# Optimization experiments

Measured on AMD Instinct MI355X. Metric: run time of the kernel, lower is better.

The kernel has to match this reference:

```python
import jax, jax.numpy as jnp
import numpy as np

N_NODES = 50000
N_EDGES = 1600000
NODE_DIM = 1024
HID = 128
OUT = 128
LN_EPS = 1e-5


def setup_inputs() -> dict:
    key = jax.random.key(0)
    ks = jax.random.split(key, 8)
    s = lambda d: 1.0 / np.sqrt(d)
    return {
        "x": jax.random.normal(ks[0], (N_NODES, NODE_DIM), jnp.float32),
        "edge_index": jax.random.randint(ks[1], (2, N_EDGES), 0, N_NODES, jnp.int64),
        "proj_w": jax.random.normal(ks[2], (HID, NODE_DIM), jnp.float32) * s(NODE_DIM),
        "proj_b": jnp.zeros((HID,), jnp.float32),
        "lin_l_w": jax.random.normal(ks[3], (HID, HID), jnp.float32) * s(HID),
        "lin_l_b": jnp.zeros((HID,), jnp.float32),
        "lin_r_w": jax.random.normal(ks[4], (HID, HID), jnp.float32) * s(HID),
        "ln_g": jnp.ones((HID,), jnp.float32),
        "ln_b": jnp.zeros((HID,), jnp.float32),
        "out_w": jax.random.normal(ks[5], (OUT, HID), jnp.float32) * s(HID),
        "out_b": jnp.zeros((OUT,), jnp.float32),
    }


def reference(x, edge_index, proj_w, proj_b, lin_l_w, lin_l_b, lin_r_w, ln_g, ln_b, out_w, out_b):
    n = x.shape[0]
    # input projection + ReLU: [N, node_dim] -> [N, H]
    h = jax.nn.relu(x @ proj_w.T + proj_b)
    # SAGEConv(mean): gather source features, mean-scatter to targets
    src, dst = edge_index[0], edge_index[1]
    agg = jax.ops.segment_sum(h[src], dst, num_segments=n)  # [N, H]
    deg = jax.ops.segment_sum(jnp.ones((src.shape[0],), h.dtype), dst, num_segments=n)
    mean_nbr = agg / jnp.maximum(deg, 1.0)[:, None]
    h = mean_nbr @ lin_l_w.T + lin_l_b + h @ lin_r_w.T
    # LayerNorm over feature dim
    mu = h.mean(-1, keepdims=True)
    var = jnp.mean((h - mu) ** 2, -1, keepdims=True)
    h = (h - mu) * jax.lax.rsqrt(var + LN_EPS) * ln_g + ln_b
    h = jax.nn.relu(h)  # dropout is identity in eval
    # batch=None -> global mean pool over all nodes: [1, H]
    g = h.mean(0, keepdims=True)
    return g @ out_w.T + out_b
```

## Files before the change

kernel.cpp:

```cpp
#include <hip/hip_runtime.h>

#define N_NODES  50000
#define N_EDGES  1600000
#define NODE_DIM 1024
#define HID      128
#define LN_EPS   1e-5f
#define NBUCK    196
#define SHARD    6250

typedef float f32x4 __attribute__((ext_vector_type(4)));
typedef __bf16 bf16x8 __attribute__((ext_vector_type(8)));
typedef unsigned short u16x8 __attribute__((ext_vector_type(8)));

__device__ __forceinline__ unsigned short f2bf(float f) {
  __bf16 b = (__bf16)f;
  return __builtin_bit_cast(unsigned short, b);
}
__device__ __forceinline__ unsigned int pkbf(float a, float b) {
  return (unsigned int)f2bf(a) | ((unsigned int)f2bf(b) << 16);
}
__device__ __forceinline__ float bf2f(unsigned short v) {
  return __uint_as_float((unsigned int)v << 16);
}

__device__ __forceinline__ int scan256_excl(int v, int buf[2][256], int t) {
  int cur = 0;
  buf[0][t] = v;
  __syncthreads();
  for (int off = 1; off < 256; off <<= 1) {
    int nxt = cur ^ 1;
    int s = buf[cur][t];
    if (t >= off) s += buf[cur][t - off];
    buf[nxt][t] = s;
    cur = nxt;
    __syncthreads();
  }
  return buf[cur][t] - v;
}

__global__ __launch_bounds__(256) void k_proj(const float* __restrict__ x,
                                              const float* __restrict__ pw,
                                              const float* __restrict__ pb,
                                              unsigned short* __restrict__ h) {
  __shared__ unsigned short As[2][128][32];
  __shared__ unsigned short Bs[2][128][32];
  const int tid = threadIdx.x;
  const int m0 = blockIdx.x * 128;
  const int wave = tid >> 6, lane = tid & 63;
  const int wm = (wave >> 1) * 64, wn = (wave & 1) * 64;
  const int srow = tid >> 1;
  const int sub  = tid & 1;
  const int fr = lane & 15, ko = (lane >> 4) * 8;

  f32x4 acc[4][4] = {};
  const int arow = m0 + srow;
  const bool aval = (arow < N_NODES);
  const float* xrow = x + (size_t)arow * NODE_DIM + sub * 32;
  const float* brow = pw + (size_t)srow * NODE_DIM + sub * 32;

  for (int k0 = 0; k0 < NODE_DIM; k0 += 64) {
    float4 av[8], bv[8];
    if (aval) {
      const float4* p = (const float4*)(xrow + k0);
#pragma unroll
      for (int j = 0; j < 8; j++) av[j] = p[j];
    } else {
#pragma unroll
      for (int j = 0; j < 8; j++) av[j] = make_float4(0.f, 0.f, 0.f, 0.f);
    }
    const float4* q = (const float4*)(brow + k0);
#pragma unroll
    for (int j = 0; j < 8; j++) bv[j] = q[j];

    __syncthreads();
    unsigned int* da = (unsigned int*)&As[sub][srow][0];
    unsigned int* db = (unsigned int*)&Bs[sub][srow][0];
#pragma unroll
    for (int j = 0; j < 8; j++) {
      da[2 * j]     = pkbf(av[j].x, av[j].y);
      da[2 * j + 1] = pkbf(av[j].z, av[j].w);
      db[2 * j]     = pkbf(bv[j].x, bv[j].y);
      db[2 * j + 1] = pkbf(bv[j].z, bv[j].w);
    }
    __syncthreads();

#pragma unroll
    for (int s = 0; s < 2; s++) {
      bf16x8 af[4], bfr[4];
#pragma unroll
      for (int m = 0; m < 4; m++)
        af[m] = *(const bf16x8*)&As[s][wm + m * 16 + fr][ko];
#pragma unroll
      for (int n = 0; n < 4; n++)
        bfr[n] = *(const bf16x8*)&Bs[s][wn + n * 16 + fr][ko];
#pragma unroll
      for (int m = 0; m < 4; m++)
#pragma unroll
        for (int n = 0; n < 4; n++)
          acc[m][n] = __builtin_amdgcn_mfma_f32_16x16x32_bf16(af[m], bfr[n], acc[m][n], 0, 0, 0);
    }
  }

  const int cr = (lane >> 4) * 4, cc = lane & 15;
#pragma unroll
  for (int n = 0; n < 4; n++) {
    const int col = wn + n * 16 + cc;
    const float bias = pb[col];
#pragma unroll
    for (int m = 0; m < 4; m++) {
#pragma unroll
      for (int i = 0; i < 4; i++) {
        const int row = m0 + wm + m * 16 + cr + i;
        if (row < N_NODES) {
          float v = acc[m][n][i] + bias;
          h[(size_t)row * HID + col] = f2bf(v > 0.f ? v : 0.f);
        }
      }
    }
  }
}

__global__ __launch_bounds__(256) void k_hist(const int* __restrict__ ei,
                                              int* __restrict__ counts) {
  __shared__ int bins[NBUCK];
  int t = threadIdx.x;
  if (t < NBUCK) bins[t] = 0;
  __syncthreads();
  int base = blockIdx.x * SHARD;
  for (int i = t; i < SHARD; i += 256)
    atomicAdd(&bins[ei[N_EDGES + base + i] >> 8], 1);
  __syncthreads();
  if (t < NBUCK) counts[t * 256 + blockIdx.x] = bins[t];
}

__global__ __launch_bounds__(256) void k_s1(const int* __restrict__ counts,
                                            int* __restrict__ basem,
                                            int* __restrict__ btot) {
  __shared__ int buf[2][256];
  int t = threadIdx.x, b = blockIdx.x;
  int v = counts[b * 256 + t];
  int excl = scan256_excl(v, buf, t);
  basem[b * 256 + t] = excl;
  if (t == 255) btot[b] = excl + v;
}

__global__ __launch_bounds__(256) void k_s2(const int* __restrict__ btot,
                                            int* __restrict__ bstart,
                                            float* __restrict__ accum) {
  __shared__ int buf[2][256];
  int t = threadIdx.x;
  int v = (t < NBUCK) ? btot[t] : 0;
  int excl = scan256_excl(v, buf, t);
  if (t < NBUCK) bstart[t] = excl;
  if (t == 0) bstart[NBUCK] = N_EDGES;
  if (t < HID) accum[t] = 0.f;
}

__global__ __launch_bounds__(256) void k_scatter(const int* __restrict__ ei,
                                                 const int* __restrict__ basem,
                                                 const int* __restrict__ bstart,
                                                 unsigned int* __restrict__ bs) {
  __shared__ int cur[NBUCK];
  int t = threadIdx.x;
  if (t < NBUCK) cur[t] = bstart[t] + basem[t * 256 + blockIdx.x];
  __syncthreads();
  int base = blockIdx.x * SHARD;
  for (int i = t; i < SHARD; i += 256) {
    int e = base + i;
    unsigned int src = (unsigned int)ei[e];
    unsigned int dst = (unsigned int)ei[N_EDGES + e];
    int pos = atomicAdd(&cur[dst >> 8], 1);
    bs[pos] = src | ((dst & 255u) << 16);
  }
}

__global__ __launch_bounds__(256) void k_bucket(const int* __restrict__ bstart,
                                                const unsigned int* __restrict__ bs,
                                                unsigned short* __restrict__ nbr,
                                                int* __restrict__ offs,
                                                int* __restrict__ deg) {
  __shared__ int bins[256];
  __shared__ int buf[2][256];
  __shared__ int curs[256];
  int t = threadIdx.x, b = blockIdx.x;
  int s = bstart[b], e = bstart[b + 1];
  bins[t] = 0;
  __syncthreads();
  for (int i = s + t; i < e; i += 256)
    atomicAdd(&bins[(bs[i] >> 16) & 255u], 1);
  __syncthreads();
  int v = bins[t];
  int excl = scan256_excl(v, buf, t);
  int node = b * 256 + t;
  deg[node]  = v;
  offs[node] = s + excl;
  curs[t]    = s + excl;
  __syncthreads();
  for (int i = s + t; i < e; i += 256) {
    unsigned int p = bs[i];
    int pos = atomicAdd(&curs[(p >> 16) & 255u], 1);
    nbr[pos] = (unsigned short)(p & 0xffffu);
  }
}

__global__ __launch_bounds__(256) void k_gather(const unsigned short* __restrict__ h,
                                                const unsigned short* __restrict__ nbr,
                                                const int* __restrict__ offs,
                                                const int* __restrict__ deg,
                                                unsigned short* __restrict__ mn) {
  const int wave = threadIdx.x >> 6;
  const int lane = threadIdx.x & 63;
  const int node = blockIdx.x * 4 + wave;
  if (node >= N_NODES) return;
  const int g = lane >> 4, li = lane & 15;
  const int d  = deg[node];
  const int st = offs[node];
  float a[8] = {0.f, 0.f, 0.f, 0.f, 0.f, 0.f, 0.f, 0.f};
  int n = g;
  for (; n + 4 < d; n += 8) {
    int s0 = nbr[st + n];
    int s1 = nbr[st + n + 4];
    u16x8 v0 = *(const u16x8*)(h + (size_t)s0 * HID + li * 8);
    u16x8 v1 = *(const u16x8*)(h + (size_t)s1 * HID + li * 8);
#pragma unroll
    for (int k = 0; k < 8; k++) a[k] += bf2f(v0[k]) + bf2f(v1[k]);
  }
  if (n < d) {
    int s0 = nbr[st + n];
    u16x8 v0 = *(const u16x8*)(h + (size_t)s0 * HID + li * 8);
#pragma unroll
    for (int k = 0; k < 8; k++) a[k] += bf2f(v0[k]);
  }
#pragma unroll
  for (int k = 0; k < 8; k++) {
    a[k] += __shfl_xor(a[k], 16);
    a[k] += __shfl_xor(a[k], 32);
  }
  if (g == 0) {
    float inv = 1.f / fmaxf((float)d, 1.f);
    u16x8 r;
#pragma unroll
    for (int k = 0; k < 8; k++) r[k] = f2bf(a[k] * inv);
    *(u16x8*)(mn + (size_t)node * HID + li * 8) = r;
  }
}

__global__ __launch_bounds__(256) void k_sage(const unsigned short* __restrict__ mn,
                                              const unsigned short* __restrict__ h,
                                              const float* __restrict__ wl,
                                              const float* __restrict__ wr,
                                              const float* __restrict__ lb,
                                              const float* __restrict__ lg,
                                              const float* __restrict__ lbt,
                                              float* __restrict__ accum) {
  __shared__ unsigned short As[128 * 32];
  __shared__ unsigned short Bs[128 * 32];
  __shared__ float T3[32 * 128];
  __shared__ float red[4][128];
  const int tid = threadIdx.x;
  const int m0 = blockIdx.x * 128;
  const int wave = tid >> 6, lane = tid & 63;
  const int wm = (wave >> 1) * 64, wn = (wave & 1) * 64;
  const int srow = tid >> 1, scol = (tid & 1) * 16;
  const int fr = lane & 15, ko = (lane >> 4) * 8;

  f32x4 acc[4][4] = {};

  for (int k0 = 0; k0 < 2 * HID; k0 += 32) {
    const unsigned short* baseA = (k0 < HID) ? mn : h;
    const float* baseB = (k0 < HID) ? wl : wr;
    const int kk = (k0 & (HID - 1)) + scol;
    const int arow = m0 + srow;
    u16x8 a0 = {0, 0, 0, 0, 0, 0, 0, 0}, a1 = a0;
    if (arow < N_NODES) {
      const u16x8* p = (const u16x8*)(baseA + (size_t)arow * HID + kk);
      a0 = p[0]; a1 = p[1];
    }
    const float4* q = (const float4*)(baseB + (size_t)srow * HID + kk);
    float4 b0 = q[0], b1 = q[1], b2 = q[2], b3 = q[3];

    __syncthreads();
    *(u16x8*)&As[srow * 32 + scol]     = a0;
    *(u16x8*)&As[srow * 32 + scol + 8] = a1;
    unsigned int* db = (unsigned int*)&Bs[srow * 32 + scol];
    db[0] = pkbf(b0.x, b0.y); db[1] = pkbf(b0.z, b0.w);
    db[2] = pkbf(b1.x, b1.y); db[3] = pkbf(b1.z, b1.w);
    db[4] = pkbf(b2.x, b2.y); db[5] = pkbf(b2.z, b2.w);
    db[6] = pkbf(b3.x, b3.y); db[7] = pkbf(b3.z, b3.w);
    __syncthreads();

    bf16x8 af[4], bfr[4];
#pragma unroll
    for (int m = 0; m < 4; m++)
      af[m] = *(const bf16x8*)&As[(wm + m * 16 + fr) * 32 + ko];
#pragma unroll
    for (int n = 0; n < 4; n++)
      bfr[n] = *(const bf16x8*)&Bs[(wn + n * 16 + fr) * 32 + ko];
#pragma unroll
    for (int m = 0; m < 4; m++)
#pragma unroll
      for (int n = 0; n < 4; n++)
        acc[m][n] = __builtin_amdgcn_mfma_f32_16x16x32_bf16(af[m], bfr[n], acc[m][n], 0, 0, 0);
  }

  const int cr = (lane >> 4) * 4, cc = lane & 15;
  const int p = wave >> 1;
  const float g0 = lg[lane], g1 = lg[lane + 64];
  const float t0 = lbt[lane], t1 = lbt[lane + 64];
  float ax = 0.f, ay = 0.f;
#pragma unroll
  for (int m = 0; m < 4; m++) {
    __syncthreads();
#pragma unroll
    for (int n = 0; n < 4; n++) {
      const int col = wn + n * 16 + cc;
      const float bias = lb[col];
#pragma unroll
      for (int i = 0; i < 4; i++)
        T3[(p * 16 + cr + i) * 128 + col] = acc[m][n][i] + bias;
    }
    __syncthreads();
    for (int r8 = 0; r8 < 8; r8++) {
      int q8 = wave * 8 + r8;
      int grow = m0 + (q8 >> 4) * 64 + m * 16 + (q8 & 15);
      float v0 = T3[q8 * 128 + lane];
      float v1 = T3[q8 * 128 + lane + 64];
      float sum = v0 + v1, ss = v0 * v0 + v1 * v1;
#pragma unroll
      for (int off = 32; off > 0; off >>= 1) {
        sum += __shfl_xor(sum, off);
        ss  += __shfl_xor(ss, off);
      }
      float mu  = sum * (1.f / HID);
      float var = ss * (1.f / HID) - mu * mu;
      float rinv = rsqrtf(var + LN_EPS);
      if (grow < N_NODES) {
        float y0 = (v0 - mu) * rinv * g0 + t0;
        float y1 = (v1 - mu) * rinv * g1 + t1;
        ax += fmaxf(y0, 0.f);
        ay += fmaxf(y1, 0.f);
      }
    }
  }
  red[wave][lane]      = ax;
  red[wave][lane + 64] = ay;
  __syncthreads();
  if (wave == 0) {
    float a  = red[0][lane] + red[1][lane] + red[2][lane] + red[3][lane];
    float bb = red[0][lane + 64] + red[1][lane + 64] + red[2][lane + 64] + red[3][lane + 64];
    atomicAdd(&accum[lane], a);
    atomicAdd(&accum[lane + 64], bb);
  }
}

__global__ __launch_bounds__(128) void k_final(const float* __restrict__ accum,
                                               const float* __restrict__ ow,
                                               const float* __restrict__ ob,
                                               float* __restrict__ out) {
  __shared__ float gs[HID];
  int t = threadIdx.x;
  gs[t] = accum[t] * (1.f / N_NODES);
  __syncthreads();
  float s = ob[t];
  for (int k = 0; k < HID; k++) s += gs[k] * ow[t * HID + k];
  out[t] = s;
}

extern "C" void kernel_launch(void* const* d_in, const int* in_sizes, int n_in,
                              void* d_out, int out_size, void* d_ws, size_t ws_size,
                              hipStream_t stream) {
  const float* x   = (const float*)d_in[0];
  const int*   ei  = (const int*)d_in[1];
  const float* pw  = (const float*)d_in[2];
  const float* pb  = (const float*)d_in[3];
  const float* wl  = (const float*)d_in[4];
  const float* lb  = (const float*)d_in[5];
  const float* wr  = (const float*)d_in[6];
  const float* lg  = (const float*)d_in[7];
  const float* lbt = (const float*)d_in[8];
  const float* ow  = (const float*)d_in[9];
  const float* ob  = (const float*)d_in[10];
  float* out = (float*)d_out;

  const int PAD = NBUCK * 256;
  unsigned short* h  = (unsigned short*)d_ws;
  unsigned short* mn = h + (size_t)PAD * HID;
  unsigned int* bsp  = (unsigned int*)(mn + (size_t)PAD * HID);
  unsigned short* nbr = (unsigned short*)(bsp + N_EDGES);
  int* counts = (int*)(nbr + N_EDGES);
  int* basem  = counts + NBUCK * 256;
  int* btot   = basem + NBUCK * 256;
  int* bstart = btot + 256;
  int* offs   = bstart + 256;
  int* deg    = offs + PAD;
  float* accum = (float*)(deg + PAD);

  const int MB = (N_NODES + 127) / 128;

  hipLaunchKernelGGL(k_proj,    dim3(MB),    dim3(256), 0, stream, x, pw, pb, h);
  hipLaunchKernelGGL(k_hist,    dim3(256),   dim3(256), 0, stream, ei, counts);
  hipLaunchKernelGGL(k_s1,      dim3(NBUCK), dim3(256), 0, stream, counts, basem, btot);
  hipLaunchKernelGGL(k_s2,      dim3(1),     dim3(256), 0, stream, btot, bstart, accum);
  hipLaunchKernelGGL(k_scatter, dim3(256),   dim3(256), 0, stream, ei, basem, bstart, bsp);
  hipLaunchKernelGGL(k_bucket,  dim3(NBUCK), dim3(256), 0, stream, bstart, bsp, nbr, offs, deg);
  hipLaunchKernelGGL(k_gather,  dim3((N_NODES + 3) / 4), dim3(256), 0, stream, h, nbr, offs, deg, mn);
  hipLaunchKernelGGL(k_sage,    dim3(MB),    dim3(256), 0, stream, mn, h, wl, wr, lb, lg, lbt, accum);
  hipLaunchKernelGGL(k_final,   dim3(1),     dim3(128), 0, stream, accum, ow, ob, out);
}
```

Baseline: 474.0 us.

## Pre-convert weights to bf16 and drop LDS staging in projection and SAGE GEMMs

Adds a prep kernel that converts the projection weight and the concatenated lin_l/lin_r weights to bf16 once per call. The projection and SAGE GEMMs now load MFMA fragments straight from global memory into registers, with each wave owning 32 rows by 128 columns, so the LDS staging and barriers go away. LayerNorm is computed in registers using shuffle reductions instead of an LDS transpose. The pooling atomics are replaced by per-block partial sums that k_final reduces. The risk is that each wave must fetch its whole B operand from L2 or L1 with no LDS sharing, and x rows are loaded as narrower 32-byte pieces per lane.

```diff
diff --git a/kernel.cpp b/kernel.cpp
--- a/kernel.cpp
+++ b/kernel.cpp
@@ -7,6 +7,7 @@
 #define LN_EPS   1e-5f
 #define NBUCK    196
 #define SHARD    6250
+#define MB       391
 
 typedef float f32x4 __attribute__((ext_vector_type(4)));
 typedef __bf16 bf16x8 __attribute__((ext_vector_type(8)));
@@ -21,6 +22,12 @@
 }
 __device__ __forceinline__ float bf2f(unsigned short v) {
   return __uint_as_float((unsigned int)v << 16);
+}
+__device__ __forceinline__ bf16x8 cvt8(const float4 a, const float4 b) {
+  union { unsigned int u[4]; bf16x8 v; } t;
+  t.u[0] = pkbf(a.x, a.y); t.u[1] = pkbf(a.z, a.w);
+  t.u[2] = pkbf(b.x, b.y); t.u[3] = pkbf(b.z, b.w);
+  return t.v;
 }
 
 __device__ __forceinline__ int scan256_excl(int v, int buf[2][256], int t) {
@@ -38,82 +45,75 @@
   return buf[cur][t] - v;
 }
 
+__global__ __launch_bounds__(256) void k_prep(const float* __restrict__ pw,
+                                              const float* __restrict__ wl,
+                                              const float* __restrict__ wr,
+                                              unsigned short* __restrict__ pwb,
+                                              unsigned short* __restrict__ wcomb) {
+  int i = blockIdx.x * 256 + threadIdx.x;
+  if (i < HID * NODE_DIM) {
+    pwb[i] = f2bf(pw[i]);
+  } else {
+    int j = i - HID * NODE_DIM;
+    if (j < HID * 256) {
+      int c = j >> 8, k = j & 255;
+      float v = (k < HID) ? wl[c * HID + k] : wr[c * HID + (k - HID)];
+      wcomb[j] = f2bf(v);
+    }
+  }
+}
+
 __global__ __launch_bounds__(256) void k_proj(const float* __restrict__ x,
-                                              const float* __restrict__ pw,
+                                              const unsigned short* __restrict__ pwb,
                                               const float* __restrict__ pb,
                                               unsigned short* __restrict__ h) {
-  __shared__ unsigned short As[2][128][32];
-  __shared__ unsigned short Bs[2][128][32];
-  const int tid = threadIdx.x;
-  const int m0 = blockIdx.x * 128;
-  const int wave = tid >> 6, lane = tid & 63;
-  const int wm = (wave >> 1) * 64, wn = (wave & 1) * 64;
-  const int srow = tid >> 1;
-  const int sub  = tid & 1;
-  const int fr = lane & 15, ko = (lane >> 4) * 8;
-
-  f32x4 acc[4][4] = {};
-  const int arow = m0 + srow;
-  const bool aval = (arow < N_NODES);
-  const float* xrow = x + (size_t)arow * NODE_DIM + sub * 32;
-  const float* brow = pw + (size_t)srow * NODE_DIM + sub * 32;
-
-  for (int k0 = 0; k0 < NODE_DIM; k0 += 64) {
-    float4 av[8], bv[8];
-    if (aval) {
-      const float4* p = (const float4*)(xrow + k0);
-#pragma unroll
-      for (int j = 0; j < 8; j++) av[j] = p[j];
-    } else {
-#pragma unroll
-      for (int j = 0; j < 8; j++) av[j] = make_float4(0.f, 0.f, 0.f, 0.f);
-    }
-    const float4* q = (const float4*)(brow + k0);
-#pragma unroll
-    for (int j = 0; j < 8; j++) bv[j] = q[j];
-
-    __syncthreads();
-    unsigned int* da = (unsigned int*)&As[sub][srow][0];
-    unsigned int* db = (unsigned int*)&Bs[sub][srow][0];
-#pragma unroll
-    for (int j = 0; j < 8; j++) {
-      da[2 * j]     = pkbf(av[j].x, av[j].y);
-      da[2 * j + 1] = pkbf(av[j].z, av[j].w);
-      db[2 * j]     = pkbf(bv[j].x, bv[j].y);
-      db[2 * j + 1] = pkbf(bv[j].z, bv[j].w);
-    }
-    __syncthreads();
-
-#pragma unroll
-    for (int s = 0; s < 2; s++) {
-      bf16x8 af[4], bfr[4];
-#pragma unroll
-      for (int m = 0; m < 4; m++)
-        af[m] = *(const bf16x8*)&As[s][wm + m * 16 + fr][ko];
-#pragma unroll
-      for (int n = 0; n < 4; n++)
-        bfr[n] = *(const bf16x8*)&Bs[s][wn + n * 16 + fr][ko];
-#pragma unroll
-      for (int m = 0; m < 4; m++)
-#pragma unroll
-        for (int n = 0; n < 4; n++)
-          acc[m][n] = __builtin_amdgcn_mfma_f32_16x16x32_bf16(af[m], bfr[n], acc[m][n], 0, 0, 0);
-    }
-  }
-
-  const int cr = (lane >> 4) * 4, cc = lane & 15;
-#pragma unroll
-  for (int n = 0; n < 4; n++) {
-    const int col = wn + n * 16 + cc;
-    const float bias = pb[col];
-#pragma unroll
-    for (int m = 0; m < 4; m++) {
-#pragma unroll
-      for (int i = 0; i < 4; i++) {
-        const int row = m0 + wm + m * 16 + cr + i;
-        if (row < N_NODES) {
-          float v = acc[m][n][i] + bias;
-          h[(size_t)row * HID + col] = f2bf(v > 0.f ? v : 0.f);
+  const int wave = threadIdx.x >> 6, lane = threadIdx.x & 63;
+  const int wr0 = blockIdx.x * 128 + wave * 32;
+  const int fr = lane & 15, kg = lane >> 4;
+
+  int r0 = wr0 + fr;       if (r0 > N_NODES - 1) r0 = N_NODES - 1;
+  int r1 = wr0 + 16 + fr;  if (r1 > N_NODES - 1) r1 = N_NODES - 1;
+  const float* pA0 = x + (size_t)r0 * NODE_DIM + kg * 8;
+  const float* pA1 = x + (size_t)r1 * NODE_DIM + kg * 8;
+  const unsigned short* pB[8];
+#pragma unroll
+  for (int n = 0; n < 8; n++)
+    pB[n] = pwb + (size_t)(n * 16 + fr) * NODE_DIM + kg * 8;
+
+  f32x4 acc[2][8] = {};
+
+#pragma unroll 2
+  for (int k0 = 0; k0 < NODE_DIM; k0 += 32) {
+    float4 a00 = *(const float4*)(pA0 + k0);
+    float4 a01 = *(const float4*)(pA0 + k0 + 4);
+    float4 a10 = *(const float4*)(pA1 + k0);
+    float4 a11 = *(const float4*)(pA1 + k0 + 4);
+    bf16x8 bfv[8];
+#pragma unroll
+    for (int n = 0; n < 8; n++) bfv[n] = *(const bf16x8*)(pB[n] + k0);
+    bf16x8 af0 = cvt8(a00, a01);
+    bf16x8 af1 = cvt8(a10, a11);
+#pragma unroll
+    for (int n = 0; n < 8; n++) {
+      acc[0][n] = __builtin_amdgcn_mfma_f32_16x16x32_bf16(af0, bfv[n], acc[0][n], 0, 0, 0);
+      acc[1][n] = __builtin_amdgcn_mfma_f32_16x16x32_bf16(af1, bfv[n], acc[1][n], 0, 0, 0);
+    }
+  }
+
+  float pbv[8];
+#pragma unroll
+  for (int n = 0; n < 8; n++) pbv[n] = pb[n * 16 + fr];
+
+#pragma unroll
+  for (int m = 0; m < 2; m++) {
+#pragma unroll
+    for (int i = 0; i < 4; i++) {
+      const int row = wr0 + m * 16 + kg * 4 + i;
+      if (row < N_NODES) {
+#pragma unroll
+        for (int n = 0; n < 8; n++) {
+          float v = acc[m][n][i] + pbv[n];
+          h[(size_t)row * HID + n * 16 + fr] = f2bf(v > 0.f ? v : 0.f);
         }
       }
     }
@@ -145,15 +145,13 @@
 }
 
 __global__ __launch_bounds__(256) void k_s2(const int* __restrict__ btot,
-                                            int* __restrict__ bstart,
-                                            float* __restrict__ accum) {
+                                            int* __restrict__ bstart) {
   __shared__ int buf[2][256];
   int t = threadIdx.x;
   int v = (t < NBUCK) ? btot[t] : 0;
   int excl = scan256_excl(v, buf, t);
   if (t < NBUCK) bstart[t] = excl;
   if (t == 0) bstart[NBUCK] = N_EDGES;
-  if (t < HID) accum[t] = 0.f;
 }
 
 __global__ __launch_bounds__(256) void k_scatter(const int* __restrict__ ei,
@@ -247,123 +245,117 @@
 
 __global__ __launch_bounds__(256) void k_sage(const unsigned short* __restrict__ mn,
                                               const unsigned short* __restrict__ h,
-                                              const float* __restrict__ wl,
-                                              const float* __restrict__ wr,
+                                              const unsigned short* __restrict__ wcomb,
                                               const float* __restrict__ lb,
                                               const float* __restrict__ lg,
                                               const float* __restrict__ lbt,
-                                              float* __restrict__ accum) {
-  __shared__ unsigned short As[128 * 32];
-  __shared__ unsigned short Bs[128 * 32];
-  __shared__ float T3[32 * 128];
+                                              float* __restrict__ part) {
   __shared__ float red[4][128];
-  const int tid = threadIdx.x;
-  const int m0 = blockIdx.x * 128;
-  const int wave = tid >> 6, lane = tid & 63;
-  const int wm = (wave >> 1) * 64, wn = (wave & 1) * 64;
-  const int srow = tid >> 1, scol = (tid & 1) * 16;
-  const int fr = lane & 15, ko = (lane >> 4) * 8;
-
-  f32x4 acc[4][4] = {};
-
-  for (int k0 = 0; k0 < 2 * HID; k0 += 32) {
+  const int wave = threadIdx.x >> 6, lane = threadIdx.x & 63;
+  const int wr0 = blockIdx.x * 128 + wave * 32;
+  const int fr = lane & 15, kg = lane >> 4;
+
+  int r0 = wr0 + fr;       if (r0 > N_NODES - 1) r0 = N_NODES - 1;
+  int r1 = wr0 + 16 + fr;  if (r1 > N_NODES - 1) r1 = N_NODES - 1;
+  const size_t o0 = (size_t)r0 * HID + kg * 8;
+  const size_t o1 = (size_t)r1 * HID + kg * 8;
+  const unsigned short* pB[8];
+#pragma unroll
+  for (int n = 0; n < 8; n++)
+    pB[n] = wcomb + (size_t)(n * 16 + fr) * 256 + kg * 8;
+
+  f32x4 acc[2][8] = {};
+
+#pragma unroll
+  for (int ks = 0; ks < 8; ks++) {
+    const int k0 = ks * 32;
     const unsigned short* baseA = (k0 < HID) ? mn : h;
-    const float* baseB = (k0 < HID) ? wl : wr;
-    const int kk = (k0 & (HID - 1)) + scol;
-    const int arow = m0 + srow;
-    u16x8 a0 = {0, 0, 0, 0, 0, 0, 0, 0}, a1 = a0;
-    if (arow < N_NODES) {
-      const u16x8* p = (const u16x8*)(baseA + (size_t)arow * HID + kk);
-      a0 = p[0]; a1 = p[1];
-    }
-    const float4* q = (const float4*)(baseB + (size_t)srow * HID + kk);
-    float4 b0 = q[0], b1 = q[1], b2 = q[2], b3 = q[3];
-
-    __syncthreads();
-    *(u16x8*)&As[srow * 32 + scol]     = a0;
-    *(u16x8*)&As[srow * 32 + scol + 8] = a1;
-    unsigned int* db = (unsigned int*)&Bs[srow * 32 + scol];
-    db[0] = pkbf(b0.x, b0.y); db[1] = pkbf(b0.z, b0.w);
-    db[2] = pkbf(b1.x, b1.y); db[3] = pkbf(b1.z, b1.w);
-    db[4] = pkbf(b2.x, b2.y); db[5] = pkbf(b2.z, b2.w);
-    db[6] = pkbf(b3.x, b3.y); db[7] = pkbf(b3.z, b3.w);
-    __syncthreads();
-
-    bf16x8 af[4], bfr[4];
-#pragma unroll
-    for (int m = 0; m < 4; m++)
-      af[m] = *(const bf16x8*)&As[(wm + m * 16 + fr) * 32 + ko];
-#pragma unroll
-    for (int n = 0; n < 4; n++)
-      bfr[n] = *(const bf16x8*)&Bs[(wn + n * 16 + fr) * 32 + ko];
-#pragma unroll
-    for (int m = 0; m < 4; m++)
-#pragma unroll
-      for (int n = 0; n < 4; n++)
-        acc[m][n] = __builtin_amdgcn_mfma_f32_16x16x32_bf16(af[m], bfr[n], acc[m][n], 0, 0, 0);
-  }
-
-  const int cr = (lane >> 4) * 4, cc = lane & 15;
-  const int p = wave >> 1;
-  const float g0 = lg[lane], g1 = lg[lane + 64];
-  const float t0 = lbt[lane], t1 = lbt[lane + 64];
-  float ax = 0.f, ay = 0.f;
-#pragma unroll
-  for (int m = 0; m < 4; m++) {
-    __syncthreads();
-#pragma unroll
-    for (int n = 0; n < 4; n++) {
-      const int col = wn + n * 16 + cc;
-      const float bias = lb[col];
-#pragma unroll
-      for (int i = 0; i < 4; i++)
-        T3[(p * 16 + cr + i) * 128 + col] = acc[m][n][i] + bias;
-    }
-    __syncthreads();
-    for (int r8 = 0; r8 < 8; r8++) {
-      int q8 = wave * 8 + r8;
-      int grow = m0 + (q8 >> 4) * 64 + m * 16 + (q8 & 15);
-      float v0 = T3[q8 * 128 + lane];
-      float v1 = T3[q8 * 128 + lane + 64];
-      float sum = v0 + v1, ss = v0 * v0 + v1 * v1;
-#pragma unroll
-      for (int off = 32; off > 0; off >>= 1) {
-        sum += __shfl_xor(sum, off);
-        ss  += __shfl_xor(ss, off);
+    const int kk = k0 & (HID - 1);
+    bf16x8 af0 = *(const bf16x8*)(baseA + o0 + kk);
+    bf16x8 af1 = *(const bf16x8*)(baseA + o1 + kk);
+    bf16x8 bfv[8];
+#pragma unroll
+    for (int n = 0; n < 8; n++) bfv[n] = *(const bf16x8*)(pB[n] + k0);
+#pragma unroll
+    for (int n = 0; n < 8; n++) {
+      acc[0][n] = __builtin_amdgcn_mfma_f32_16x16x32_bf16(af0, bfv[n], acc[0][n], 0, 0, 0);
+      acc[1][n] = __builtin_amdgcn_mfma_f32_16x16x32_bf16(af1, bfv[n], acc[1][n], 0, 0, 0);
+    }
+  }
+
+  float lbv[8], lgv[8], lbtv[8];
+#pragma unroll
+  for (int n = 0; n < 8; n++) {
+    lbv[n]  = lb[n * 16 + fr];
+    lgv[n]  = lg[n * 16 + fr];
+    lbtv[n] = lbt[n * 16 + fr];
+  }
+
+  float pool[8] = {};
+#pragma unroll
+  for (int m = 0; m < 2; m++) {
+    float ps[4] = {}, pss[4] = {};
+#pragma unroll
+    for (int n = 0; n < 8; n++)
+#pragma unroll
+      for (int i = 0; i < 4; i++) {
+        float v = acc[m][n][i] + lbv[n];
+        ps[i] += v;
+        pss[i] += v * v;
       }
-      float mu  = sum * (1.f / HID);
-      float var = ss * (1.f / HID) - mu * mu;
-      float rinv = rsqrtf(var + LN_EPS);
+#pragma unroll
+    for (int i = 0; i < 4; i++) {
+#pragma unroll
+      for (int off = 1; off < 16; off <<= 1) {
+        ps[i]  += __shfl_xor(ps[i], off);
+        pss[i] += __shfl_xor(pss[i], off);
+      }
+    }
+#pragma unroll
+    for (int i = 0; i < 4; i++) {
+      const int grow = wr0 + m * 16 + kg * 4 + i;
+      const float mu = ps[i] * (1.f / HID);
+      const float var = pss[i] * (1.f / HID) - mu * mu;
+      const float rinv = rsqrtf(var + LN_EPS);
       if (grow < N_NODES) {
-        float y0 = (v0 - mu) * rinv * g0 + t0;
-        float y1 = (v1 - mu) * rinv * g1 + t1;
-        ax += fmaxf(y0, 0.f);
-        ay += fmaxf(y1, 0.f);
+#pragma unroll
+        for (int n = 0; n < 8; n++) {
+          float v = acc[m][n][i] + lbv[n];
+          float y = (v - mu) * rinv * lgv[n] + lbtv[n];
+          pool[n] += fmaxf(y, 0.f);
+        }
       }
     }
   }
-  red[wave][lane]      = ax;
-  red[wave][lane + 64] = ay;
-  __syncthreads();
-  if (wave == 0) {
-    float a  = red[0][lane] + red[1][lane] + red[2][lane] + red[3][lane];
-    float bb = red[0][lane + 64] + red[1][lane + 64] + red[2][lane + 64] + red[3][lane + 64];
-    atomicAdd(&accum[lane], a);
-    atomicAdd(&accum[lane + 64], bb);
-  }
-}
-
-__global__ __launch_bounds__(128) void k_final(const float* __restrict__ accum,
+#pragma unroll
+  for (int n = 0; n < 8; n++) {
+    pool[n] += __shfl_xor(pool[n], 16);
+    pool[n] += __shfl_xor(pool[n], 32);
+  }
+  if (kg == 0) {
+#pragma unroll
+    for (int n = 0; n < 8; n++) red[wave][n * 16 + fr] = pool[n];
+  }
+  __syncthreads();
+  const int t = threadIdx.x;
+  if (t < 128)
+    part[(size_t)blockIdx.x * 128 + t] =
+        red[0][t] + red[1][t] + red[2][t] + red[3][t];
+}
+
+__global__ __launch_bounds__(128) void k_final(const float* __restrict__ part,
                                                const float* __restrict__ ow,
                                                const float* __restrict__ ob,
                                                float* __restrict__ out) {
   __shared__ float gs[HID];
   int t = threadIdx.x;
-  gs[t] = accum[t] * (1.f / N_NODES);
-  __syncthreads();
-  float s = ob[t];
-  for (int k = 0; k < HID; k++) s += gs[k] * ow[t * HID + k];
-  out[t] = s;
+  float s = 0.f;
+  for (int b = 0; b < MB; b++) s += part[(size_t)b * 128 + t];
+  gs[t] = s * (1.f / N_NODES);
+  __syncthreads();
+  float o = ob[t];
+  for (int k = 0; k < HID; k++) o += gs[k] * ow[t * HID + k];
+  out[t] = o;
 }
 
 extern "C" void kernel_launch(void* const* d_in, const int* in_sizes, int n_in,
@@ -383,27 +375,28 @@
   float* out = (float*)d_out;
 
   const int PAD = NBUCK * 256;
-  unsigned short* h  = (unsigned short*)d_ws;
-  unsigned short* mn = h + (size_t)PAD * HID;
-  unsigned int* bsp  = (unsigned int*)(mn + (size_t)PAD * HID);
-  unsigned short* nbr = (unsigned short*)(bsp + N_EDGES);
-  int* counts = (int*)(nbr + N_EDGES);
+  unsigned short* h    = (unsigned short*)d_ws;
+  unsigned short* mn   = h + (size_t)PAD * HID;
+  unsigned int* bsp    = (unsigned int*)(mn + (size_t)PAD * HID);
+  unsigned short* nbr  = (unsigned short*)(bsp + N_EDGES);
+  unsigned short* pwb  = nbr + N_EDGES;
+  unsigned short* wcomb= pwb + HID * NODE_DIM;
+  int* counts = (int*)(wcomb + HID * 256);
   int* basem  = counts + NBUCK * 256;
   int* btot   = basem + NBUCK * 256;
   int* bstart = btot + 256;
   int* offs   = bstart + 256;
   int* deg    = offs + PAD;
-  float* accum = (float*)(deg + PAD);
-
-  const int MB = (N_NODES + 127) / 128;
-
-  hipLaunchKernelGGL(k_proj,    dim3(MB),    dim3(256), 0, stream, x, pw, pb, h);
+  float* part = (float*)(deg + PAD);
+
+  hipLaunchKernelGGL(k_prep,    dim3(640),   dim3(256), 0, stream, pw, wl, wr, pwb, wcomb);
+  hipLaunchKernelGGL(k_proj,    dim3(MB),    dim3(256), 0, stream, x, pwb, pb, h);
   hipLaunchKernelGGL(k_hist,    dim3(256),   dim3(256), 0, stream, ei, counts);
   hipLaunchKernelGGL(k_s1,      dim3(NBUCK), dim3(256), 0, stream, counts, basem, btot);
-  hipLaunchKernelGGL(k_s2,      dim3(1),     dim3(256), 0, stream, btot, bstart, accum);
+  hipLaunchKernelGGL(k_s2,      dim3(1),     dim3(256), 0, stream, btot, bstart);
   hipLaunchKernelGGL(k_scatter, dim3(256),   dim3(256), 0, stream, ei, basem, bstart, bsp);
   hipLaunchKernelGGL(k_bucket,  dim3(NBUCK), dim3(256), 0, stream, bstart, bsp, nbr, offs, deg);
   hipLaunchKernelGGL(k_gather,  dim3((N_NODES + 3) / 4), dim3(256), 0, stream, h, nbr, offs, deg, mn);
-  hipLaunchKernelGGL(k_sage,    dim3(MB),    dim3(256), 0, stream, mn, h, wl, wr, lb, lg, lbt, accum);
-  hipLaunchKernelGGL(k_final,   dim3(1),     dim3(128), 0, stream, accum, ow, ob, out);
-}
+  hipLaunchKernelGGL(k_sage,    dim3(MB),    dim3(256), 0, stream, mn, h, wcomb, lb, lg, lbt, part);
+  hipLaunchKernelGGL(k_final,   dim3(1),     dim3(128), 0, stream, part, ow, ob, out);
+}
```

New measurement: 490.1 us. +3.4%, slower.
